# Kernel tuning notes

Hardware: AMD Instinct MI355X
Metric: run time of the kernel (lower is better)

## Reference

```python
import jax, jax.numpy as jnp
import numpy as np

B, S, D = 8, 1024, 512
H, Q, V = 8, 64, 64
NEG_INF = -2.0**32 + 1.0  # faithful to the TF module's mask fill value


def setup_inputs() -> dict:
    key = jax.random.key(0)
    ks = jax.random.split(key, 9)
    s = lambda fan_in: 1.0 / np.sqrt(fan_in)
    return {
        "x": jax.random.normal(ks[0], (B, S, D), dtype=jnp.float32),
        "Wq": jax.random.normal(ks[1], (D, Q * H), dtype=jnp.float32) * s(D),
        "bq": jnp.zeros((Q * H,), dtype=jnp.float32),
        "Wk": jax.random.normal(ks[2], (D, Q * H), dtype=jnp.float32) * s(D),
        "bk": jnp.zeros((Q * H,), dtype=jnp.float32),
        "Wv": jax.random.normal(ks[3], (D, V * H), dtype=jnp.float32) * s(D),
        "bv": jnp.zeros((V * H,), dtype=jnp.float32),
        "Wo": jax.random.normal(ks[4], (V * H, D), dtype=jnp.float32) * s(V * H),
        "bo": jnp.zeros((D,), dtype=jnp.float32),
    }


def _split_heads(t, hd):
    # [B,S,h*hd] -> split along last axis into h, concat along axis0 -> [h*B,S,hd]
    b, seq, _ = t.shape
    return t.reshape(b, seq, H, hd).transpose(2, 0, 1, 3).reshape(H * b, seq, hd)


def reference(x, Wq, bq, Wk, bk, Wv, bv, Wo, bo):
    q = _split_heads(x @ Wq + bq, Q)  # [h*B, S, q]
    k = _split_heads(x @ Wk + bk, Q)  # [h*B, S, q]
    v = _split_heads(x @ Wv + bv, V)  # [h*B, S, v]

    score = jnp.einsum("nsq,ntq->nst", q, k)  # [h*B, S, S], NOTE: no 1/sqrt(d) scaling (faithful)
    heatmap_score = score

    # stage == 'train': causal mask, masked entries set to -2^32 + 1
    mask = jnp.tril(jnp.ones((S, S), dtype=bool))
    score = jnp.where(mask, score, jnp.full_like(score, NEG_INF))
    attn = jax.nn.softmax(score, axis=-1)

    wv = jnp.einsum("nst,ntv->nsv", attn, v)  # [h*B, S, v]
    # split along axis0 into h, concat along last axis -> [B, S, h*v]
    wv = wv.reshape(H, B, S, V).transpose(1, 2, 0, 3).reshape(B, S, H * V)
    out = wv @ Wo + bo  # [B, S, D]
    return (out, heatmap_score)
```

## Files before the change

kernel.cpp:

```cpp
#include <hip/hip_runtime.h>


typedef unsigned short u16;
typedef unsigned int u32;
typedef __attribute__((ext_vector_type(8))) short bf8;
typedef __attribute__((ext_vector_type(4))) float f4;

__device__ __forceinline__ u16 f2bf(float f) {
    u32 x = __builtin_bit_cast(u32, f);
    return (u16)((x + 0x7FFFu + ((x >> 16) & 1u)) >> 16);
}

#define MFMA16(a, b, c) __builtin_amdgcn_mfma_f32_16x16x32_bf16((a), (b), (c), 0, 0, 0)

__global__ __launch_bounds__(256) void k_cvt_x(const float4* __restrict__ xi,
                                               ushort4* __restrict__ xo)
{
    int idx = blockIdx.x * 256 + threadIdx.x;
    for (int i = idx; i < 1048576; i += 262144) {
        float4 f = xi[i];
        ushort4 o;
        o.x = f2bf(f.x); o.y = f2bf(f.y); o.z = f2bf(f.z); o.w = f2bf(f.w);
        xo[i] = o;
    }
}

__global__ __launch_bounds__(256) void k_cvt_wT(
    const float* __restrict__ Wq, const float* __restrict__ Wk,
    const float* __restrict__ Wv, const float* __restrict__ Wo,
    u16* __restrict__ WqT, u16* __restrict__ WkT,
    u16* __restrict__ WvT, u16* __restrict__ WoT)
{
    const int z = blockIdx.z;
    const float* __restrict__ W = (z == 0) ? Wq : (z == 1) ? Wk : (z == 2) ? Wv : Wo;
    u16* __restrict__ WT        = (z == 0) ? WqT : (z == 1) ? WkT : (z == 2) ? WvT : WoT;

    __shared__ __align__(16) u16 Ts[64 * 72];
    const int k0 = blockIdx.x * 64, c0 = blockIdx.y * 64;
    const int tid = threadIdx.x;
    const int r = tid >> 4, cc = (tid & 15) * 4;
    #pragma unroll
    for (int rr = r; rr < 64; rr += 16) {
        float4 f = *(const float4*)&W[(size_t)(k0 + rr) * 512 + c0 + cc];
        Ts[(cc + 0) * 72 + rr] = f2bf(f.x);
        Ts[(cc + 1) * 72 + rr] = f2bf(f.y);
        Ts[(cc + 2) * 72 + rr] = f2bf(f.z);
        Ts[(cc + 3) * 72 + rr] = f2bf(f.w);
    }
    __syncthreads();
    #pragma unroll
    for (int i = 0; i < 2; ++i) {
        int gi = tid + i * 256;
        int cr = gi >> 3, g = gi & 7;
        bf8 v = *(bf8*)&Ts[cr * 72 + g * 8];
        *(bf8*)&WT[(size_t)(c0 + cr) * 512 + k0 + g * 8] = v;
    }
}

__global__ __launch_bounds__(256) void k_qkv(
    const u16* __restrict__ xb,
    const u16* __restrict__ WqT, const u16* __restrict__ WkT, const u16* __restrict__ WvT,
    const float* __restrict__ bq, const float* __restrict__ bk, const float* __restrict__ bv,
    u16* __restrict__ qb, u16* __restrict__ kb, u16* __restrict__ vT)
{
    const int which = blockIdx.z;
    const u16* __restrict__ WT     = (which == 0) ? WqT : (which == 1) ? WkT : WvT;
    const float* __restrict__ bias = (which == 0) ? bq : (which == 1) ? bk : bv;

    const int colTile = blockIdx.x * 128;
    const int rowTile = blockIdx.y * 128;

    __shared__ __align__(16) u16 As[128 * 72];
    __shared__ __align__(16) u16 Bs[128 * 72];

    const int tid = threadIdx.x;
    const int lane = tid & 63, w = tid >> 6;
    const int lm = lane & 15, kq = lane >> 4;
    const int mB = (w >> 1) * 64, nB = (w & 1) * 64;

    f4 acc[4][4] = {};

    for (int k0 = 0; k0 < 512; k0 += 64) {
        __syncthreads();
        #pragma unroll
        for (int i = 0; i < 4; ++i) {
            int gi = tid + i * 256;
            int r = gi >> 3, c = gi & 7;
            *(bf8*)&As[r * 72 + c * 8] = *(const bf8*)&xb[(size_t)(rowTile + r) * 512 + k0 + c * 8];
            *(bf8*)&Bs[r * 72 + c * 8] = *(const bf8*)&WT[(size_t)(colTile + r) * 512 + k0 + c * 8];
        }
        __syncthreads();
        #pragma unroll
        for (int ks = 0; ks < 2; ++ks) {
            bf8 a[4], b[4];
            #pragma unroll
            for (int mi = 0; mi < 4; ++mi) a[mi] = *(bf8*)&As[(mB + mi * 16 + lm) * 72 + ks * 32 + kq * 8];
            #pragma unroll
            for (int ni = 0; ni < 4; ++ni) b[ni] = *(bf8*)&Bs[(nB + ni * 16 + lm) * 72 + ks * 32 + kq * 8];
            #pragma unroll
            for (int mi = 0; mi < 4; ++mi)
                #pragma unroll
                for (int ni = 0; ni < 4; ++ni)
                    acc[mi][ni] = MFMA16(a[mi], b[ni], acc[mi][ni]);
        }
    }

    if (which < 2) {
        u16* __restrict__ outp = (which == 0) ? qb : kb;
        #pragma unroll
        for (int mi = 0; mi < 4; ++mi) {
            const int r0 = rowTile + mB + mi * 16 + kq * 4;
            #pragma unroll
            for (int ni = 0; ni < 4; ++ni) {
                const int c = colTile + nB + ni * 16 + lm;
                const float bv_ = bias[c];
                const int h = c >> 6, hd = c & 63;
                #pragma unroll
                for (int rg = 0; rg < 4; ++rg) {
                    const int rr = r0 + rg;
                    const int b = rr >> 10, s = rr & 1023;
                    outp[(size_t)(((h * 8 + b) << 10) + s) * 64 + hd] = f2bf(acc[mi][ni][rg] + bv_);
                }
            }
        }
    } else {
        #pragma unroll
        for (int mi = 0; mi < 4; ++mi) {
            const int r0 = rowTile + mB + mi * 16 + kq * 4;
            const int b = r0 >> 10, s0 = r0 & 1023;
            #pragma unroll
            for (int ni = 0; ni < 4; ++ni) {
                const int c = colTile + nB + ni * 16 + lm;
                const float bv_ = bias[c];
                const int h = c >> 6, hd = c & 63;
                ushort4 pk;
                pk.x = f2bf(acc[mi][ni][0] + bv_);
                pk.y = f2bf(acc[mi][ni][1] + bv_);
                pk.z = f2bf(acc[mi][ni][2] + bv_);
                pk.w = f2bf(acc[mi][ni][3] + bv_);
                *(ushort4*)&vT[(size_t)((h * 8 + b) * 64 + hd) * 1024 + s0] = pk;
            }
        }
    }
}

__global__ __launch_bounds__(256) void k_attn(
    const u16* __restrict__ qb, const u16* __restrict__ kb, const u16* __restrict__ vT,
    float* __restrict__ heat, u16* __restrict__ wvb)
{
    const int n = blockIdx.x;
    const int sT = blockIdx.y;
    const int s0 = sT * 128;

    __shared__ __align__(16) u16 KPs[128 * 136];
    __shared__ __align__(16) u16 Vs[64 * 136];

    const int tid = threadIdx.x;
    const int lane = tid & 63, w = tid >> 6;
    const int lm = lane & 15, kq = lane >> 4;
    const int mB = w * 32;

    const u16* __restrict__ qn = qb + (size_t)n * 65536;
    const u16* __restrict__ kn = kb + (size_t)n * 65536;
    const u16* __restrict__ vn = vT + (size_t)n * 65536;
    float* __restrict__ hp = heat + ((size_t)n << 20);

    bf8 aq[2][2];
    #pragma unroll
    for (int mi = 0; mi < 2; ++mi)
        #pragma unroll
        for (int ks = 0; ks < 2; ++ks)
            aq[mi][ks] = *(const bf8*)&qn[(size_t)(s0 + mB + mi * 16 + lm) * 64 + ks * 32 + kq * 8];

    f4 accO[2][4] = {};
    float m_i[2][4], l_i[2][4];
    #pragma unroll
    for (int mi = 0; mi < 2; ++mi)
        #pragma unroll
        for (int rg = 0; rg < 4; ++rg) { m_i[mi][rg] = -3.0e38f; l_i[mi][rg] = 0.f; }

    for (int tt = 0; tt < 8; ++tt) {
        const int t0 = tt * 128;
        const bool causal = (tt <= sT);

        __syncthreads();
        #pragma unroll
        for (int i = 0; i < 4; ++i) {
            int gi = tid + i * 256;
            int r = gi >> 3, c = gi & 7;
            *(bf8*)&KPs[r * 136 + c * 8] = *(const bf8*)&kn[(size_t)(t0 + r) * 64 + c * 8];
        }
        if (causal) {
            #pragma unroll
            for (int i = 0; i < 4; ++i) {
                int gi = tid + i * 256;
                int r = gi >> 4, g = gi & 15;
                *(bf8*)&Vs[r * 136 + g * 8] = *(const bf8*)&vn[(size_t)r * 1024 + t0 + g * 8];
            }
        }
        __syncthreads();

        f4 accS[2][8] = {};
        #pragma unroll
        for (int ks = 0; ks < 2; ++ks) {
            bf8 b[8];
            #pragma unroll
            for (int ni = 0; ni < 8; ++ni) b[ni] = *(bf8*)&KPs[(ni * 16 + lm) * 136 + ks * 32 + kq * 8];
            #pragma unroll
            for (int mi = 0; mi < 2; ++mi)
                #pragma unroll
                for (int ni = 0; ni < 8; ++ni)
                    accS[mi][ni] = MFMA16(aq[mi][ks], b[ni], accS[mi][ni]);
        }

        #pragma unroll
        for (int mi = 0; mi < 2; ++mi) {
            #pragma unroll
            for (int rg = 0; rg < 4; ++rg) {
                float* rowp = &hp[(size_t)(s0 + mB + mi * 16 + kq * 4 + rg) * 1024 + t0 + lm];
                #pragma unroll
                for (int ni = 0; ni < 8; ++ni) rowp[ni * 16] = accS[mi][ni][rg];
            }
        }

        if (causal) {
            __syncthreads();
            const bool diag = (tt == sT);
            #pragma unroll
            for (int mi = 0; mi < 2; ++mi) {
                #pragma unroll
                for (int rg = 0; rg < 4; ++rg) {
                    const int srow = s0 + mB + mi * 16 + kq * 4 + rg;
                    float tm = -3.0e38f;
                    #pragma unroll
                    for (int ni = 0; ni < 8; ++ni) {
                        float sv = accS[mi][ni][rg];
                        if (diag && (t0 + ni * 16 + lm > srow)) sv = -3.0e38f;
                        tm = fmaxf(tm, sv);
                    }
                    tm = fmaxf(tm, __shfl_xor(tm, 1));
                    tm = fmaxf(tm, __shfl_xor(tm, 2));
                    tm = fmaxf(tm, __shfl_xor(tm, 4));
                    tm = fmaxf(tm, __shfl_xor(tm, 8));
                    const float mn = fmaxf(m_i[mi][rg], tm);
                    const float alpha = __expf(m_i[mi][rg] - mn);
                    float rs = 0.f;
                    #pragma unroll
                    for (int ni = 0; ni < 8; ++ni) {
                        float sv = accS[mi][ni][rg];
                        const bool ok = !diag || (t0 + ni * 16 + lm <= srow);
                        float p = ok ? __expf(sv - mn) : 0.f;
                        rs += p;
                        KPs[(mB + mi * 16 + kq * 4 + rg) * 136 + ni * 16 + lm] = f2bf(p);
                    }
                    rs += __shfl_xor(rs, 1);
                    rs += __shfl_xor(rs, 2);
                    rs += __shfl_xor(rs, 4);
                    rs += __shfl_xor(rs, 8);
                    l_i[mi][rg] = l_i[mi][rg] * alpha + rs;
                    m_i[mi][rg] = mn;
                    #pragma unroll
                    for (int vni = 0; vni < 4; ++vni) accO[mi][vni][rg] *= alpha;
                }
            }
            __syncthreads();

            #pragma unroll
            for (int ks = 0; ks < 4; ++ks) {
                bf8 a[2], b[4];
                #pragma unroll
                for (int mi = 0; mi < 2; ++mi) a[mi] = *(bf8*)&KPs[(mB + mi * 16 + lm) * 136 + ks * 32 + kq * 8];
                #pragma unroll
                for (int vni = 0; vni < 4; ++vni) b[vni] = *(bf8*)&Vs[(vni * 16 + lm) * 136 + ks * 32 + kq * 8];
                #pragma unroll
                for (int mi = 0; mi < 2; ++mi)
                    #pragma unroll
                    for (int vni = 0; vni < 4; ++vni)
                        accO[mi][vni] = MFMA16(a[mi], b[vni], accO[mi][vni]);
            }
        }
    }

    u16* __restrict__ wn = wvb + (size_t)n * 65536;
    #pragma unroll
    for (int mi = 0; mi < 2; ++mi) {
        #pragma unroll
        for (int rg = 0; rg < 4; ++rg) {
            const float li = 1.0f / l_i[mi][rg];
            const int s = s0 + mB + mi * 16 + kq * 4 + rg;
            #pragma unroll
            for (int vni = 0; vni < 4; ++vni)
                wn[(size_t)s * 64 + vni * 16 + lm] = f2bf(accO[mi][vni][rg] * li);
        }
    }
}

__global__ __launch_bounds__(256) void k_out(
    const u16* __restrict__ wvb, const u16* __restrict__ WoT, const float* __restrict__ bo,
    float* __restrict__ outp)
{
    const int colTile = blockIdx.x * 128;
    const int rowTile = blockIdx.y * 128;
    const int b = rowTile >> 10, s0 = rowTile & 1023;

    __shared__ __align__(16) u16 As[128 * 72];
    __shared__ __align__(16) u16 Bs[128 * 72];

    const int tid = threadIdx.x;
    const int lane = tid & 63, w = tid >> 6;
    const int lm = lane & 15, kq = lane >> 4;
    const int mB = (w >> 1) * 64, nB = (w & 1) * 64;

    f4 acc[4][4] = {};

    for (int k0 = 0; k0 < 512; k0 += 64) {
        const int h = k0 >> 6;
        const u16* __restrict__ abase = wvb + (size_t)((h * 8 + b) * 1024 + s0) * 64;
        __syncthreads();
        #pragma unroll
        for (int i = 0; i < 4; ++i) {
            int gi = tid + i * 256;
            int r = gi >> 3, c = gi & 7;
            *(bf8*)&As[r * 72 + c * 8] = *(const bf8*)&abase[(size_t)r * 64 + c * 8];
            *(bf8*)&Bs[r * 72 + c * 8] = *(const bf8*)&WoT[(size_t)(colTile + r) * 512 + k0 + c * 8];
        }
        __syncthreads();
        #pragma unroll
        for (int ks = 0; ks < 2; ++ks) {
            bf8 a[4], b2[4];
            #pragma unroll
            for (int mi = 0; mi < 4; ++mi) a[mi] = *(bf8*)&As[(mB + mi * 16 + lm) * 72 + ks * 32 + kq * 8];
            #pragma unroll
            for (int ni = 0; ni < 4; ++ni) b2[ni] = *(bf8*)&Bs[(nB + ni * 16 + lm) * 72 + ks * 32 + kq * 8];
            #pragma unroll
            for (int mi = 0; mi < 4; ++mi)
                #pragma unroll
                for (int ni = 0; ni < 4; ++ni)
                    acc[mi][ni] = MFMA16(a[mi], b2[ni], acc[mi][ni]);
        }
    }

    #pragma unroll
    for (int mi = 0; mi < 4; ++mi) {
        const int r0 = rowTile + mB + mi * 16 + kq * 4;
        #pragma unroll
        for (int ni = 0; ni < 4; ++ni) {
            const int c = colTile + nB + ni * 16 + lm;
            const float bv_ = bo[c];
            #pragma unroll
            for (int rg = 0; rg < 4; ++rg)
                outp[(size_t)(r0 + rg) * 512 + c] = acc[mi][ni][rg] + bv_;
        }
    }
}

extern "C" void kernel_launch(void* const* d_in, const int* in_sizes, int n_in,
                              void* d_out, int out_size, void* d_ws, size_t ws_size,
                              hipStream_t stream)
{
    (void)in_sizes; (void)n_in; (void)out_size; (void)ws_size;

    const float* x  = (const float*)d_in[0];
    const float* Wq = (const float*)d_in[1];
    const float* bq = (const float*)d_in[2];
    const float* Wk = (const float*)d_in[3];
    const float* bk = (const float*)d_in[4];
    const float* Wv = (const float*)d_in[5];
    const float* bv = (const float*)d_in[6];
    const float* Wo = (const float*)d_in[7];
    const float* bo = (const float*)d_in[8];

    float* outp = (float*)d_out;
    float* heat = outp + 4194304;

    u16* ws16 = (u16*)d_ws;
    u16* xb  = ws16;
    u16* WqT = xb  + 4194304;
    u16* WkT = WqT + 262144;
    u16* WvT = WkT + 262144;
    u16* WoT = WvT + 262144;
    u16* qb  = WoT + 262144;
    u16* kb  = qb  + 4194304;
    u16* vT  = kb  + 4194304;
    u16* wvb = vT  + 4194304;

    k_cvt_x <<<1024, 256, 0, stream>>>((const float4*)x, (ushort4*)xb);
    k_cvt_wT<<<dim3(8, 8, 4), 256, 0, stream>>>(Wq, Wk, Wv, Wo, WqT, WkT, WvT, WoT);
    k_qkv   <<<dim3(4, 64, 3), 256, 0, stream>>>(xb, WqT, WkT, WvT, bq, bk, bv, qb, kb, vT);
    k_attn  <<<dim3(64, 8), 256, 0, stream>>>(qb, kb, vT, heat, wvb);
    k_out   <<<dim3(4, 64), 256, 0, stream>>>(wvb, WoT, bo, outp);
}
```

Before: 395.3 us.

## Load GEMM and attention tiles straight into LDS with XOR swizzle; reorder attention blocks

Replaces register-staged global→LDS copies in the QKV, attention and output kernels with direct global-to-LDS loads (`global_load_lds`). Drops the padded LDS layout in favour of an XOR-swizzled unpadded one to avoid bank conflicts. The attention grid is flattened to 1D so the heaviest causal row tiles are scheduled first for better load balance, and one barrier before the P·V stage is removed. The lost barrier relies on each wave reading only its own P rows, and the swizzle index maths must match between writes and reads.

```diff
diff --git a/kernel.cpp b/kernel.cpp
--- a/kernel.cpp
+++ b/kernel.cpp
@@ -12,6 +12,10 @@
 }
 
 #define MFMA16(a, b, c) __builtin_amdgcn_mfma_f32_16x16x32_bf16((a), (b), (c), 0, 0, 0)
+
+#define GLD16(gp, lp) __builtin_amdgcn_global_load_lds( \
+    (const __attribute__((address_space(1))) unsigned int*)(gp), \
+    (__attribute__((address_space(3))) unsigned int*)(lp), 16, 0, 0)
 
 __global__ __launch_bounds__(256) void k_cvt_x(const float4* __restrict__ xi,
                                                ushort4* __restrict__ xo)
@@ -70,33 +74,37 @@
     const int colTile = blockIdx.x * 128;
     const int rowTile = blockIdx.y * 128;
 
-    __shared__ __align__(16) u16 As[128 * 72];
-    __shared__ __align__(16) u16 Bs[128 * 72];
+    __shared__ __align__(16) u16 As[128 * 64];
+    __shared__ __align__(16) u16 Bs[128 * 64];
 
     const int tid = threadIdx.x;
     const int lane = tid & 63, w = tid >> 6;
     const int lm = lane & 15, kq = lane >> 4;
     const int mB = (w >> 1) * 64, nB = (w & 1) * 64;
 
+    const int sr = lane >> 3;
+    const int sg = (lane & 7) ^ sr;
+
     f4 acc[4][4] = {};
 
     for (int k0 = 0; k0 < 512; k0 += 64) {
         __syncthreads();
         #pragma unroll
         for (int i = 0; i < 4; ++i) {
-            int gi = tid + i * 256;
-            int r = gi >> 3, c = gi & 7;
-            *(bf8*)&As[r * 72 + c * 8] = *(const bf8*)&xb[(size_t)(rowTile + r) * 512 + k0 + c * 8];
-            *(bf8*)&Bs[r * 72 + c * 8] = *(const bf8*)&WT[(size_t)(colTile + r) * 512 + k0 + c * 8];
+            const int rb = w * 32 + i * 8;
+            GLD16(&xb[(size_t)(rowTile + rb + sr) * 512 + k0 + sg * 8], &As[rb * 64]);
+            GLD16(&WT[(size_t)(colTile + rb + sr) * 512 + k0 + sg * 8], &Bs[rb * 64]);
         }
         __syncthreads();
         #pragma unroll
         for (int ks = 0; ks < 2; ++ks) {
             bf8 a[4], b[4];
             #pragma unroll
-            for (int mi = 0; mi < 4; ++mi) a[mi] = *(bf8*)&As[(mB + mi * 16 + lm) * 72 + ks * 32 + kq * 8];
-            #pragma unroll
-            for (int ni = 0; ni < 4; ++ni) b[ni] = *(bf8*)&Bs[(nB + ni * 16 + lm) * 72 + ks * 32 + kq * 8];
+            for (int mi = 0; mi < 4; ++mi)
+                a[mi] = *(bf8*)&As[(mB + mi * 16 + lm) * 64 + (((ks * 4 + kq) ^ (lm & 7)) * 8)];
+            #pragma unroll
+            for (int ni = 0; ni < 4; ++ni)
+                b[ni] = *(bf8*)&Bs[(nB + ni * 16 + lm) * 64 + (((ks * 4 + kq) ^ (lm & 7)) * 8)];
             #pragma unroll
             for (int mi = 0; mi < 4; ++mi)
                 #pragma unroll
@@ -148,18 +156,22 @@
     const u16* __restrict__ qb, const u16* __restrict__ kb, const u16* __restrict__ vT,
     float* __restrict__ heat, u16* __restrict__ wvb)
 {
-    const int n = blockIdx.x;
-    const int sT = blockIdx.y;
+    const int bid = blockIdx.x;
+    const int sT = (bid < 256) ? (7 - (bid >> 6)) : ((bid >> 6) - 4);
+    const int n = bid & 63;
     const int s0 = sT * 128;
 
     __shared__ __align__(16) u16 KPs[128 * 136];
-    __shared__ __align__(16) u16 Vs[64 * 136];
+    __shared__ __align__(16) u16 Vs[64 * 128];
 
     const int tid = threadIdx.x;
     const int lane = tid & 63, w = tid >> 6;
     const int lm = lane & 15, kq = lane >> 4;
     const int mB = w * 32;
 
+    const int sr = lane >> 3, sg = (lane & 7) ^ sr;
+    const int vr = lane >> 4, vg = lane & 15;
+
     const u16* __restrict__ qn = qb + (size_t)n * 65536;
     const u16* __restrict__ kn = kb + (size_t)n * 65536;
     const u16* __restrict__ vn = vT + (size_t)n * 65536;
@@ -186,16 +198,15 @@
         __syncthreads();
         #pragma unroll
         for (int i = 0; i < 4; ++i) {
-            int gi = tid + i * 256;
-            int r = gi >> 3, c = gi & 7;
-            *(bf8*)&KPs[r * 136 + c * 8] = *(const bf8*)&kn[(size_t)(t0 + r) * 64 + c * 8];
+            const int rb = w * 32 + i * 8;
+            GLD16(&kn[(size_t)(t0 + rb + sr) * 64 + sg * 8], &KPs[rb * 64]);
         }
         if (causal) {
             #pragma unroll
             for (int i = 0; i < 4; ++i) {
-                int gi = tid + i * 256;
-                int r = gi >> 4, g = gi & 15;
-                *(bf8*)&Vs[r * 136 + g * 8] = *(const bf8*)&vn[(size_t)r * 1024 + t0 + g * 8];
+                const int rb = w * 16 + i * 4;
+                const int r = rb + vr;
+                GLD16(&vn[(size_t)r * 1024 + t0 + ((vg ^ (r & 7)) * 8)], &Vs[rb * 128]);
             }
         }
         __syncthreads();
@@ -205,7 +216,8 @@
         for (int ks = 0; ks < 2; ++ks) {
             bf8 b[8];
             #pragma unroll
-            for (int ni = 0; ni < 8; ++ni) b[ni] = *(bf8*)&KPs[(ni * 16 + lm) * 136 + ks * 32 + kq * 8];
+            for (int ni = 0; ni < 8; ++ni)
+                b[ni] = *(bf8*)&KPs[(ni * 16 + lm) * 64 + (((ks * 4 + kq) ^ (lm & 7)) * 8)];
             #pragma unroll
             for (int mi = 0; mi < 2; ++mi)
                 #pragma unroll
@@ -263,15 +275,16 @@
                     for (int vni = 0; vni < 4; ++vni) accO[mi][vni][rg] *= alpha;
                 }
             }
-            __syncthreads();
 
             #pragma unroll
             for (int ks = 0; ks < 4; ++ks) {
                 bf8 a[2], b[4];
                 #pragma unroll
-                for (int mi = 0; mi < 2; ++mi) a[mi] = *(bf8*)&KPs[(mB + mi * 16 + lm) * 136 + ks * 32 + kq * 8];
-                #pragma unroll
-                for (int vni = 0; vni < 4; ++vni) b[vni] = *(bf8*)&Vs[(vni * 16 + lm) * 136 + ks * 32 + kq * 8];
+                for (int mi = 0; mi < 2; ++mi)
+                    a[mi] = *(bf8*)&KPs[(mB + mi * 16 + lm) * 136 + ks * 32 + kq * 8];
+                #pragma unroll
+                for (int vni = 0; vni < 4; ++vni)
+                    b[vni] = *(bf8*)&Vs[(vni * 16 + lm) * 128 + (((ks * 4 + kq) ^ (lm & 7)) * 8)];
                 #pragma unroll
                 for (int mi = 0; mi < 2; ++mi)
                     #pragma unroll
@@ -303,14 +316,17 @@
     const int rowTile = blockIdx.y * 128;
     const int b = rowTile >> 10, s0 = rowTile & 1023;
 
-    __shared__ __align__(16) u16 As[128 * 72];
-    __shared__ __align__(16) u16 Bs[128 * 72];
+    __shared__ __align__(16) u16 As[128 * 64];
+    __shared__ __align__(16) u16 Bs[128 * 64];
 
     const int tid = threadIdx.x;
     const int lane = tid & 63, w = tid >> 6;
     const int lm = lane & 15, kq = lane >> 4;
     const int mB = (w >> 1) * 64, nB = (w & 1) * 64;
 
+    const int sr = lane >> 3;
+    const int sg = (lane & 7) ^ sr;
+
     f4 acc[4][4] = {};
 
     for (int k0 = 0; k0 < 512; k0 += 64) {
@@ -319,19 +335,20 @@
         __syncthreads();
         #pragma unroll
         for (int i = 0; i < 4; ++i) {
-            int gi = tid + i * 256;
-            int r = gi >> 3, c = gi & 7;
-            *(bf8*)&As[r * 72 + c * 8] = *(const bf8*)&abase[(size_t)r * 64 + c * 8];
-            *(bf8*)&Bs[r * 72 + c * 8] = *(const bf8*)&WoT[(size_t)(colTile + r) * 512 + k0 + c * 8];
+            const int rb = w * 32 + i * 8;
+            GLD16(&abase[(size_t)(rb + sr) * 64 + sg * 8], &As[rb * 64]);
+            GLD16(&WoT[(size_t)(colTile + rb + sr) * 512 + k0 + sg * 8], &Bs[rb * 64]);
         }
         __syncthreads();
         #pragma unroll
         for (int ks = 0; ks < 2; ++ks) {
             bf8 a[4], b2[4];
             #pragma unroll
-            for (int mi = 0; mi < 4; ++mi) a[mi] = *(bf8*)&As[(mB + mi * 16 + lm) * 72 + ks * 32 + kq * 8];
-            #pragma unroll
-            for (int ni = 0; ni < 4; ++ni) b2[ni] = *(bf8*)&Bs[(nB + ni * 16 + lm) * 72 + ks * 32 + kq * 8];
+            for (int mi = 0; mi < 4; ++mi)
+                a[mi] = *(bf8*)&As[(mB + mi * 16 + lm) * 64 + (((ks * 4 + kq) ^ (lm & 7)) * 8)];
+            #pragma unroll
+            for (int ni = 0; ni < 4; ++ni)
+                b2[ni] = *(bf8*)&Bs[(nB + ni * 16 + lm) * 64 + (((ks * 4 + kq) ^ (lm & 7)) * 8)];
             #pragma unroll
             for (int mi = 0; mi < 4; ++mi)
                 #pragma unroll
@@ -387,6 +404,6 @@
     k_cvt_x <<<1024, 256, 0, stream>>>((const float4*)x, (ushort4*)xb);
     k_cvt_wT<<<dim3(8, 8, 4), 256, 0, stream>>>(Wq, Wk, Wv, Wo, WqT, WkT, WvT, WoT);
     k_qkv   <<<dim3(4, 64, 3), 256, 0, stream>>>(xb, WqT, WkT, WvT, bq, bk, bv, qb, kb, vT);
-    k_attn  <<<dim3(64, 8), 256, 0, stream>>>(qb, kb, vT, heat, wvb);
+    k_attn  <<<dim3(512), 256, 0, stream>>>(qb, kb, vT, heat, wvb);
     k_out   <<<dim3(4, 64), 256, 0, stream>>>(wvb, WoT, bo, outp);
 }
```

Result: no change. 392.0 us (-0.8%).
